# Performance work log

Measured on AMD Instinct MI355X. Metric: run time of the kernel, lower is better.

Reference implementation:

```python
import jax, jax.numpy as jnp
import numpy as np

B, N, D, WIN = 2, 4096, 256, 16


def setup_inputs() -> dict:
    key = jax.random.key(0)
    ks = jax.random.split(key, 10)
    def lin(k, o, i):
        return 0.02 * jax.random.normal(k, (o, i), jnp.float32)
    W = N // WIN
    return {
        "x": 0.5 * jax.random.normal(ks[0], (B, N, D), jnp.float32),
        "embed_qk": jax.random.normal(ks[1], (3, B, W, WIN, WIN, 3), jnp.float32),
        "act_proj_w": lin(ks[2], D, D), "act_proj_b": jnp.zeros((D,), jnp.float32),
        "proj_ln_g": jnp.ones((D,), jnp.float32), "proj_ln_b": jnp.zeros((D,), jnp.float32),
        "conv_w": lin(ks[3], D, D), "conv_b": jnp.zeros((D,), jnp.float32),
        "q_w": lin(ks[4], D, D), "q_b": jnp.zeros((D,), jnp.float32),
        "k_w": lin(ks[5], D, D), "k_b": jnp.zeros((D,), jnp.float32),
        "p_w": lin(ks[6], 1, 3), "p_b": jnp.zeros((1,), jnp.float32),
        "lin_w": lin(ks[7], D, D), "lin_b": jnp.zeros((D,), jnp.float32),
        "norm_g": jnp.ones((D,), jnp.float32), "norm_b": jnp.zeros((D,), jnp.float32),
    }


def _ln(x, g, b, eps=1e-5):
    m = x.mean(-1, keepdims=True)
    v = ((x - m) ** 2).mean(-1, keepdims=True)
    return (x - m) * jax.lax.rsqrt(v + eps) * g + b


def reference(x, embed_qk, act_proj_w, act_proj_b, proj_ln_g, proj_ln_b,
              conv_w, conv_b, q_w, q_b, k_w, k_b, p_w, p_b,
              lin_w, lin_b, norm_g, norm_b):
    # MSMAttentionLayer: gated residual path
    act_res = jax.nn.silu(x @ act_proj_w.T + act_proj_b)          # (B,N,C)
    h = _ln(x, proj_ln_g, proj_ln_b)
    h = jax.nn.silu(h @ conv_w.T + conv_b)                        # 1x1 conv == per-token linear

    # MSMLMultiHeadAttention, stage=1 (window 4x4=16); N % 16 == 0 so add_row_num = 0
    q = jax.nn.elu(h @ q_w.T + q_b) + 1.0
    k = jax.nn.elu(h @ k_w.T + k_b) + 1.0
    v = h
    Bn, Nn, C = h.shape
    Wn = Nn // WIN
    q_win = q.reshape(Bn, Wn, WIN, C)
    k_win = k.reshape(Bn, Wn, WIN, C)
    v_win = v.reshape(Bn, Wn, WIN, C)
    # learned relative-position bias: Linear(3,1) on embed_qk[stage]
    p = (embed_qk[1] @ p_w.T + p_b)[..., 0]
    # second elu+1 feature map (applied on top of q/k which are already elu+1)
    phi_q = jax.nn.elu(q_win) + 1.0
    phi_k = jax.nn.elu(k_win) + 1.0
    # linear-attention style KV aggregation: reduces over windows w
    KV = jnp.einsum('bwmc,bwmd->bmcd', phi_k, v_win)
    att = jnp.einsum('bwnc,bmcd->bwnmd', phi_q, KV) + p[..., None]
    attn_out = att.reshape(Bn, -1, C)[:, :Nn, :]                  # (B,N,C)

    hid = (attn_out * act_res) @ lin_w.T + lin_b
    return _ln(hid + h, norm_g, norm_b)
```

## Files before the change

### kernel.cpp

```cpp
#include <hip/hip_runtime.h>


#define DIM 256
#define NTOK 4096

typedef __attribute__((ext_vector_type(8))) short short8;
typedef __attribute__((ext_vector_type(4))) short short4v;
typedef __attribute__((ext_vector_type(4))) float f32x4;

__device__ __forceinline__ float silu_f(float z) { return z / (1.f + __expf(-z)); }
__device__ __forceinline__ float elu2_f(float z) { return z > 0.f ? z + 2.f : __expf(z) + 1.f; }

__device__ __forceinline__ short f2bf(float f) {
    union { float f; unsigned u; } v; v.f = f;
    unsigned r = v.u + 0x7fffu + ((v.u >> 16) & 1u);
    return (short)(r >> 16);
}
__device__ __forceinline__ float bf2f(short s) {
    union { unsigned u; float f; } v; v.u = ((unsigned)(unsigned short)s) << 16;
    return v.f;
}
__device__ __forceinline__ short8 cvt8(const float* src) {
    const float4 a = *(const float4*)src;
    const float4 c = *(const float4*)(src + 4);
    short8 s;
    s[0] = f2bf(a.x); s[1] = f2bf(a.y); s[2] = f2bf(a.z); s[3] = f2bf(a.w);
    s[4] = f2bf(c.x); s[5] = f2bf(c.y); s[6] = f2bf(c.z); s[7] = f2bf(c.w);
    return s;
}

__device__ __forceinline__ void cast_chunk(const float* __restrict__ src, short* __restrict__ dst,
                                           int chunk, int tid) {
    const int base = chunk * 8192 + tid * 32;
    #pragma unroll
    for (int j = 0; j < 4; ++j)
        *(short8*)(dst + base + j * 8) = cvt8(src + base + j * 8);
}

__global__ __launch_bounds__(256) void fused_dual(
        const float* __restrict__ XF,
        const float* __restrict__ W0f, const float* __restrict__ b0, short* __restrict__ Y0,
        const float* __restrict__ W1f, const float* __restrict__ b1, short* __restrict__ Y1,
        const float* __restrict__ G, const float* __restrict__ Bt,
        const float* __restrict__ Wkf, short* __restrict__ WKB,
        const float* __restrict__ Wqf, short* __restrict__ WQB) {
    const int tid = threadIdx.x;
    if (blockIdx.x >= 64) {
        if (blockIdx.y == 0 && blockIdx.z == 0) {
            const int which = blockIdx.x - 64;
            if (which < 8) cast_chunk(Wkf, WKB, which, tid);
            else cast_chunk(Wqf, WQB, which - 8, tid);
        }
        return;
    }
    __shared__ __align__(16) short Xs[128 * 72];
    __shared__ __align__(16) short Ws[64 * 72];
    __shared__ float stats[128][2];
    const int zz = blockIdx.z;
    const float* Wf = zz ? W1f : W0f;
    const float* bias = zz ? b1 : b0;
    short* Y = zz ? Y1 : Y0;
    const int wv = tid >> 6, l = tid & 63;
    const int lr = l & 15, lk = l >> 4;
    const int r0 = blockIdx.x * 128, c0 = blockIdx.y * 64;
    const int wm = (wv >> 1) * 64, wn = (wv & 1) * 32;

    if (zz) {
        const int prow = tid >> 1, phalf = tid & 1;
        const float* src = XF + (size_t)(r0 + prow) * DIM + phalf * 128;
        float a1 = 0.f, a2 = 0.f;
        #pragma unroll 8
        for (int j = 0; j < 32; ++j) {
            const float4 v = *(const float4*)(src + j * 4);
            a1 += v.x + v.y + v.z + v.w;
            a2 += v.x * v.x + v.y * v.y + v.z * v.z + v.w * v.w;
        }
        a1 += __shfl_xor(a1, 1);
        a2 += __shfl_xor(a2, 1);
        if (!phalf) {
            const float mm = a1 * (1.f / DIM);
            stats[prow][0] = mm;
            stats[prow][1] = rsqrtf(a2 * (1.f / DIM) - mm * mm + 1e-5f);
        }
        __syncthreads();
    }

    f32x4 acc[4][2];
    #pragma unroll
    for (int i = 0; i < 4; ++i)
        #pragma unroll
        for (int j = 0; j < 2; ++j) acc[i][j] = (f32x4){0.f, 0.f, 0.f, 0.f};
    const int sr = tid >> 3, sc = (tid & 7) * 8;
    for (int kt = 0; kt < DIM; kt += 64) {
        float gv[8], bv[8];
        if (zz) {
            const float4 g1 = *(const float4*)(G + kt + sc);
            const float4 g2 = *(const float4*)(G + kt + sc + 4);
            const float4 t1 = *(const float4*)(Bt + kt + sc);
            const float4 t2 = *(const float4*)(Bt + kt + sc + 4);
            gv[0] = g1.x; gv[1] = g1.y; gv[2] = g1.z; gv[3] = g1.w;
            gv[4] = g2.x; gv[5] = g2.y; gv[6] = g2.z; gv[7] = g2.w;
            bv[0] = t1.x; bv[1] = t1.y; bv[2] = t1.z; bv[3] = t1.w;
            bv[4] = t2.x; bv[5] = t2.y; bv[6] = t2.z; bv[7] = t2.w;
        }
        #pragma unroll
        for (int p = 0; p < 4; ++p) {
            const int row = sr + p * 32;
            const float* src = XF + (size_t)(r0 + row) * DIM + kt + sc;
            const float4 a = *(const float4*)src;
            const float4 c = *(const float4*)(src + 4);
            float v[8] = {a.x, a.y, a.z, a.w, c.x, c.y, c.z, c.w};
            short8 s;
            if (zz) {
                const float mm = stats[row][0], rs = stats[row][1];
                #pragma unroll
                for (int j = 0; j < 8; ++j) s[j] = f2bf((v[j] - mm) * rs * gv[j] + bv[j]);
            } else {
                #pragma unroll
                for (int j = 0; j < 8; ++j) s[j] = f2bf(v[j]);
            }
            *(short8*)&Xs[row * 72 + sc] = s;
        }
        #pragma unroll
        for (int p = 0; p < 2; ++p) {
            const int row = sr + p * 32;
            *(short8*)&Ws[row * 72 + sc] = cvt8(Wf + (size_t)(c0 + row) * DIM + kt + sc);
        }
        __syncthreads();
        #pragma unroll
        for (int kc = 0; kc < 2; ++kc) {
            short8 af[4], bfr[2];
            #pragma unroll
            for (int mi = 0; mi < 4; ++mi)
                af[mi] = *(const short8*)&Xs[(wm + mi * 16 + lr) * 72 + kc * 32 + lk * 8];
            #pragma unroll
            for (int ni = 0; ni < 2; ++ni)
                bfr[ni] = *(const short8*)&Ws[(wn + ni * 16 + lr) * 72 + kc * 32 + lk * 8];
            #pragma unroll
            for (int mi = 0; mi < 4; ++mi)
                #pragma unroll
                for (int ni = 0; ni < 2; ++ni)
                    acc[mi][ni] = __builtin_amdgcn_mfma_f32_16x16x32_bf16(af[mi], bfr[ni], acc[mi][ni], 0, 0, 0);
        }
        __syncthreads();
    }
    #pragma unroll
    for (int mi = 0; mi < 4; ++mi)
        #pragma unroll
        for (int ni = 0; ni < 2; ++ni) {
            const int c = c0 + wn + ni * 16 + lr;
            const float bv2 = bias[c];
            #pragma unroll
            for (int i = 0; i < 4; ++i) {
                const int r = r0 + wm + mi * 16 + lk * 4 + i;
                Y[(size_t)r * DIM + c] = f2bf(silu_f(acc[mi][ni][i] + bv2));
            }
        }
}

__global__ __launch_bounds__(256) void gemm_kq(
        const short* __restrict__ H, const short* __restrict__ WKB, const float* __restrict__ bk, short* __restrict__ PK,
        const short* __restrict__ WQB, const float* __restrict__ bq, short* __restrict__ PQ) {
    __shared__ __align__(16) short Xs[128 * 72];
    __shared__ __align__(16) short Ws[64 * 72];
    const int bx = blockIdx.x;
    const bool isq = bx >= 64;
    const short* W = isq ? WQB : WKB;
    const float* bias = isq ? bq : bk;
    short* Y = isq ? PQ : PK;
    const int r0 = (isq ? bx - 64 : bx) * 128;
    const int c0 = blockIdx.y * 64;
    const int tid = threadIdx.x;
    const int wv = tid >> 6, l = tid & 63;
    const int lr = l & 15, lk = l >> 4;
    const int wm = (wv >> 1) * 64, wn = (wv & 1) * 32;
    f32x4 acc[4][2];
    #pragma unroll
    for (int i = 0; i < 4; ++i)
        #pragma unroll
        for (int j = 0; j < 2; ++j) acc[i][j] = (f32x4){0.f, 0.f, 0.f, 0.f};
    const int sr = tid >> 3, sc = (tid & 7) * 8;
    for (int kt = 0; kt < DIM; kt += 64) {
        #pragma unroll
        for (int p = 0; p < 4; ++p) {
            const int row = sr + p * 32;
            int grow = r0 + row;
            if (isq) grow = ((grow >> 8) << 12) + (grow & 255);
            *(short8*)&Xs[row * 72 + sc] = *(const short8*)(H + (size_t)grow * DIM + kt + sc);
        }
        #pragma unroll
        for (int p = 0; p < 2; ++p) {
            const int row = sr + p * 32;
            *(short8*)&Ws[row * 72 + sc] = *(const short8*)(W + (size_t)(c0 + row) * DIM + kt + sc);
        }
        __syncthreads();
        #pragma unroll
        for (int kc = 0; kc < 2; ++kc) {
            short8 af[4], bfr[2];
            #pragma unroll
            for (int mi = 0; mi < 4; ++mi)
                af[mi] = *(const short8*)&Xs[(wm + mi * 16 + lr) * 72 + kc * 32 + lk * 8];
            #pragma unroll
            for (int ni = 0; ni < 2; ++ni)
                bfr[ni] = *(const short8*)&Ws[(wn + ni * 16 + lr) * 72 + kc * 32 + lk * 8];
            #pragma unroll
            for (int mi = 0; mi < 4; ++mi)
                #pragma unroll
                for (int ni = 0; ni < 2; ++ni)
                    acc[mi][ni] = __builtin_amdgcn_mfma_f32_16x16x32_bf16(af[mi], bfr[ni], acc[mi][ni], 0, 0, 0);
        }
        __syncthreads();
    }
    #pragma unroll
    for (int mi = 0; mi < 4; ++mi)
        #pragma unroll
        for (int ni = 0; ni < 2; ++ni) {
            const int c = c0 + wn + ni * 16 + lr;
            const float bv = bias[c];
            #pragma unroll
            for (int i = 0; i < 4; ++i) {
                const int r = r0 + wm + mi * 16 + lk * 4 + i;
                Y[(size_t)r * DIM + c] = f2bf(elu2_f(acc[mi][ni][i] + bv));
            }
        }
}

__global__ __launch_bounds__(256) void kv_mfma(const short* __restrict__ HB, const short* __restrict__ PK,
                                               short* __restrict__ KVT,
                                               const float* __restrict__ Wlf, short* __restrict__ WLB) {
    const int tid = threadIdx.x;
    if (blockIdx.x >= 32) {
        if (blockIdx.y == 0 && blockIdx.z == 0)
            cast_chunk(Wlf, WLB, blockIdx.x - 32, tid);
        return;
    }
    __shared__ __align__(16) short Hs[64 * 68];
    __shared__ __align__(16) short Ps[64 * 68];
    const int bm = blockIdx.x, b = bm >> 4, m = bm & 15;
    const int d0 = blockIdx.y * 64, c0 = blockIdx.z * 64;
    const int wv = tid >> 6, l = tid & 63;
    const int lr = l & 15, lk = l >> 4;
    const int wd = (wv >> 1) * 32, wc = (wv & 1) * 32;
    f32x4 acc[2][2];
    #pragma unroll
    for (int i = 0; i < 2; ++i)
        #pragma unroll
        for (int j = 0; j < 2; ++j) acc[i][j] = (f32x4){0.f, 0.f, 0.f, 0.f};
    const size_t hbase = (size_t)b * NTOK * DIM;
    const int sr = tid >> 3, sc = (tid & 7) * 8;
    for (int kt = 0; kt < 256; kt += 64) {
        #pragma unroll
        for (int p = 0; p < 2; ++p) {
            const int w = sr + p * 32;
            const size_t gg = hbase + (size_t)((kt + w) * 16 + m) * DIM;
            short8 hv = *(const short8*)(HB + gg + d0 + sc);
            short8 pv = *(const short8*)(PK + gg + c0 + sc);
            *(short4v*)&Hs[w * 68 + sc]     = __builtin_shufflevector(hv, hv, 0, 1, 2, 3);
            *(short4v*)&Hs[w * 68 + sc + 4] = __builtin_shufflevector(hv, hv, 4, 5, 6, 7);
            *(short4v*)&Ps[w * 68 + sc]     = __builtin_shufflevector(pv, pv, 0, 1, 2, 3);
            *(short4v*)&Ps[w * 68 + sc + 4] = __builtin_shufflevector(pv, pv, 4, 5, 6, 7);
        }
        __syncthreads();
        #pragma unroll
        for (int kc = 0; kc < 2; ++kc) {
            const int kb = kc * 32 + lk * 8;
            short8 af[2], bfr[2];
            #pragma unroll
            for (int di = 0; di < 2; ++di)
                #pragma unroll
                for (int i = 0; i < 8; ++i)
                    af[di][i] = Hs[(kb + i) * 68 + wd + di * 16 + lr];
            #pragma unroll
            for (int ci = 0; ci < 2; ++ci)
                #pragma unroll
                for (int i = 0; i < 8; ++i)
                    bfr[ci][i] = Ps[(kb + i) * 68 + wc + ci * 16 + lr];
            #pragma unroll
            for (int di = 0; di < 2; ++di)
                #pragma unroll
                for (int ci = 0; ci < 2; ++ci)
                    acc[di][ci] = __builtin_amdgcn_mfma_f32_16x16x32_bf16(af[di], bfr[ci], acc[di][ci], 0, 0, 0);
        }
        __syncthreads();
    }
    #pragma unroll
    for (int di = 0; di < 2; ++di)
        #pragma unroll
        for (int ci = 0; ci < 2; ++ci)
            #pragma unroll
            for (int i = 0; i < 4; ++i) {
                const int d = d0 + wd + di * 16 + lk * 4 + i;
                const int c = c0 + wc + ci * 16 + lr;
                KVT[((size_t)bm * DIM + d) * DIM + c] = f2bf(acc[di][ci][i]);
            }
}

__global__ __launch_bounds__(256) void attlin(
        const short* __restrict__ PQ, const short* __restrict__ KVT,
        const float* __restrict__ emb, const float* __restrict__ pw, const float* __restrict__ pb,
        const short* __restrict__ AR,
        const short* __restrict__ WLB, const float* __restrict__ bl,
        const short* __restrict__ HB, const float* __restrict__ G, const float* __restrict__ Bt,
        float* __restrict__ Y) {
    __shared__ __align__(16) short Qs[32 * 264];
    __shared__ __align__(16) short AGs[32 * 264];
    __shared__ __align__(16) short Bs[256 * 72];
    __shared__ float s1buf[32][2];
    __shared__ float s2buf[32][2];
    const int tid = threadIdx.x;
    const int wv = tid >> 6, l = tid & 63;
    const int lr = l & 15, lk = l >> 4;
    const int bm = blockIdx.x, b = bm >> 4, m = bm & 15;
    const int q0 = blockIdx.y * 32;
    const int wq = (wv >> 1) * 16;
    const int wd = (wv & 1) * 32;
    const int sr = tid >> 3, sc = (tid & 7) * 8;

    #pragma unroll
    for (int p = 0; p < 4; ++p) {
        const int chunk = tid + p * 256;
        const int row = chunk >> 5, cc = (chunk & 31) * 8;
        *(short8*)&Qs[row * 264 + cc] = *(const short8*)(PQ + (size_t)(b * 256 + q0 + row) * DIM + cc);
    }

    f32x4 accA[4][2];
    #pragma unroll
    for (int i = 0; i < 4; ++i)
        #pragma unroll
        for (int j = 0; j < 2; ++j) accA[i][j] = (f32x4){0.f, 0.f, 0.f, 0.f};
    for (int kt = 0; kt < DIM; kt += 64) {
        #pragma unroll
        for (int p = 0; p < 8; ++p) {
            const int row = sr + p * 32;
            *(short8*)&Bs[row * 72 + sc] = *(const short8*)(KVT + ((size_t)bm * DIM + row) * DIM + kt + sc);
        }
        __syncthreads();
        #pragma unroll
        for (int kc = 0; kc < 2; ++kc) {
            const short8 af = *(const short8*)&Qs[(wq + lr) * 264 + kt + kc * 32 + lk * 8];
            #pragma unroll
            for (int dc = 0; dc < 4; ++dc)
                #pragma unroll
                for (int ni = 0; ni < 2; ++ni) {
                    const short8 bfr = *(const short8*)&Bs[(dc * 64 + wd + ni * 16 + lr) * 72 + kc * 32 + lk * 8];
                    accA[dc][ni] = __builtin_amdgcn_mfma_f32_16x16x32_bf16(af, bfr, accA[dc][ni], 0, 0, 0);
                }
        }
        __syncthreads();
    }
    {
        const float pw0 = pw[0], pw1 = pw[1], pw2 = pw[2], pbv = pb[0];
        #pragma unroll
        for (int i = 0; i < 4; ++i) {
            const int rloc = wq + lk * 4 + i;
            const int qr = q0 + rloc;
            const int widx = qr >> 4, nidx = qr & 15;
            const float* e = emb + ((((size_t)(2 + b) * 256 + widx) * 16 + nidx) * 16 + m) * 3;
            const float pv = e[0] * pw0 + e[1] * pw1 + e[2] * pw2 + pbv;
            const int t = qr * 16 + m;
            #pragma unroll
            for (int dc = 0; dc < 4; ++dc)
                #pragma unroll
                for (int ni = 0; ni < 2; ++ni) {
                    const int d = dc * 64 + wd + ni * 16 + lr;
                    const size_t o = ((size_t)b * NTOK + t) * DIM + d;
                    AGs[rloc * 264 + d] = f2bf((accA[dc][ni][i] + pv) * bf2f(AR[o]));
                }
        }
    }
    __syncthreads();

    const int wn2 = (wv & 1) * 128;
    f32x4 accB[8];
    #pragma unroll
    for (int i = 0; i < 8; ++i) accB[i] = (f32x4){0.f, 0.f, 0.f, 0.f};
    for (int kt = 0; kt < DIM; kt += 64) {
        #pragma unroll
        for (int p = 0; p < 8; ++p) {
            const int row = sr + p * 32;
            *(short8*)&Bs[row * 72 + sc] = *(const short8*)(WLB + (size_t)row * DIM + kt + sc);
        }
        __syncthreads();
        #pragma unroll
        for (int kc = 0; kc < 2; ++kc) {
            const short8 af = *(const short8*)&AGs[(wq + lr) * 264 + kt + kc * 32 + lk * 8];
            #pragma unroll
            for (int ni = 0; ni < 8; ++ni) {
                const short8 bfr = *(const short8*)&Bs[(wn2 + ni * 16 + lr) * 72 + kc * 32 + lk * 8];
                accB[ni] = __builtin_amdgcn_mfma_f32_16x16x32_bf16(af, bfr, accB[ni], 0, 0, 0);
            }
        }
        __syncthreads();
    }
    float s1[4] = {0.f, 0.f, 0.f, 0.f}, s2[4] = {0.f, 0.f, 0.f, 0.f};
    #pragma unroll
    for (int ni = 0; ni < 8; ++ni) {
        const int col = wn2 + ni * 16 + lr;
        const float bv = bl[col];
        #pragma unroll
        for (int i = 0; i < 4; ++i) {
            const int rloc = wq + lk * 4 + i;
            const int t = (q0 + rloc) * 16 + m;
            const float z = accB[ni][i] + bv + bf2f(HB[((size_t)b * NTOK + t) * DIM + col]);
            accB[ni][i] = z;
            s1[i] += z; s2[i] += z * z;
        }
    }
    #pragma unroll
    for (int o = 1; o < 16; o <<= 1) {
        #pragma unroll
        for (int i = 0; i < 4; ++i) {
            s1[i] += __shfl_xor(s1[i], o);
            s2[i] += __shfl_xor(s2[i], o);
        }
    }
    if (lr == 0) {
        #pragma unroll
        for (int i = 0; i < 4; ++i) {
            const int rloc = wq + lk * 4 + i;
            s1buf[rloc][wv & 1] = s1[i];
            s2buf[rloc][wv & 1] = s2[i];
        }
    }
    __syncthreads();
    float mean[4], rstd[4];
    #pragma unroll
    for (int i = 0; i < 4; ++i) {
        const int rloc = wq + lk * 4 + i;
        const float t1 = s1buf[rloc][0] + s1buf[rloc][1];
        const float t2 = s2buf[rloc][0] + s2buf[rloc][1];
        const float mm = t1 * (1.f / DIM);
        mean[i] = mm;
        rstd[i] = rsqrtf(t2 * (1.f / DIM) - mm * mm + 1e-5f);
    }
    #pragma unroll
    for (int ni = 0; ni < 8; ++ni) {
        const int col = wn2 + ni * 16 + lr;
        const float gv = G[col], bv2 = Bt[col];
        #pragma unroll
        for (int i = 0; i < 4; ++i) {
            const int rloc = wq + lk * 4 + i;
            const int t = (q0 + rloc) * 16 + m;
            Y[((size_t)b * NTOK + t) * DIM + col] = (accB[ni][i] - mean[i]) * rstd[i] * gv + bv2;
        }
    }
}

extern "C" void kernel_launch(void* const* d_in, const int* in_sizes, int n_in,
                              void* d_out, int out_size, void* d_ws, size_t ws_size,
                              hipStream_t stream) {
    const float* x   = (const float*)d_in[0];
    const float* emb = (const float*)d_in[1];
    const float* Wa  = (const float*)d_in[2];
    const float* ba  = (const float*)d_in[3];
    const float* lng = (const float*)d_in[4];
    const float* lnb = (const float*)d_in[5];
    const float* Wc  = (const float*)d_in[6];
    const float* bc  = (const float*)d_in[7];
    const float* Wq  = (const float*)d_in[8];
    const float* bq  = (const float*)d_in[9];
    const float* Wk  = (const float*)d_in[10];
    const float* bk  = (const float*)d_in[11];
    const float* pw  = (const float*)d_in[12];
    const float* pb  = (const float*)d_in[13];
    const float* Wl  = (const float*)d_in[14];
    const float* bl  = (const float*)d_in[15];
    const float* ng  = (const float*)d_in[16];
    const float* nb  = (const float*)d_in[17];

    char* ws = (char*)d_ws;
    const size_t MB = 1024 * 1024;
    short* h_bf   = (short*)(ws + 0 * MB);
    short* phik   = (short*)(ws + 4 * MB);
    short* phiq   = (short*)(ws + 8 * MB);
    short* kvT    = (short*)(ws + 9 * MB);
    short* act_bf = (short*)(ws + 13 * MB);
    short* Wk_bf  = (short*)(ws + 17 * MB);
    short* Wq_bf  = (short*)(ws + 17 * MB + 128 * 1024);
    short* Wl_bf  = (short*)(ws + 17 * MB + 256 * 1024);

    fused_dual<<<dim3(80, 4, 2), dim3(256), 0, stream>>>(x, Wa, ba, act_bf,
                                                         Wc, bc, h_bf, lng, lnb,
                                                         Wk, Wk_bf, Wq, Wq_bf);
    gemm_kq<<<dim3(68, 4), dim3(256), 0, stream>>>(h_bf, Wk_bf, bk, phik, Wq_bf, bq, phiq);
    kv_mfma<<<dim3(40, 4, 4), dim3(256), 0, stream>>>(h_bf, phik, kvT, Wl, Wl_bf);
    attlin<<<dim3(32, 8), dim3(256), 0, stream>>>(phiq, kvT, emb, pw, pb, act_bf, Wl_bf, bl,
                                                  h_bf, ng, nb, (float*)d_out);
}
```

Baseline: 56.61 us.

## Fuse K and Q projections into KV and attention kernels, drop gemm_kq launch

Removes the separate gemm_kq kernel. phi_k is now computed inside the KV aggregation kernel from shared-memory H tiles and a resident Wk slice, and phi_q is computed at the start of the attention kernel. The Wl bf16 cast moves into the first kernel, so there is one fewer launch and no phi_k/phi_q round trip through global memory. In exchange, kv_fused recomputes the K projection once per d-half (grid z=2) and uses much more shared memory, which may reduce occupancy.

```diff
diff --git a/kernel.cpp b/kernel.cpp
--- a/kernel.cpp
+++ b/kernel.cpp
@@ -28,7 +28,6 @@
     s[4] = f2bf(c.x); s[5] = f2bf(c.y); s[6] = f2bf(c.z); s[7] = f2bf(c.w);
     return s;
 }
-
 __device__ __forceinline__ void cast_chunk(const float* __restrict__ src, short* __restrict__ dst,
                                            int chunk, int tid) {
     const int base = chunk * 8192 + tid * 32;
@@ -43,13 +42,15 @@
         const float* __restrict__ W1f, const float* __restrict__ b1, short* __restrict__ Y1,
         const float* __restrict__ G, const float* __restrict__ Bt,
         const float* __restrict__ Wkf, short* __restrict__ WKB,
-        const float* __restrict__ Wqf, short* __restrict__ WQB) {
+        const float* __restrict__ Wqf, short* __restrict__ WQB,
+        const float* __restrict__ Wlf, short* __restrict__ WLB) {
     const int tid = threadIdx.x;
     if (blockIdx.x >= 64) {
         if (blockIdx.y == 0 && blockIdx.z == 0) {
             const int which = blockIdx.x - 64;
             if (which < 8) cast_chunk(Wkf, WKB, which, tid);
-            else cast_chunk(Wqf, WQB, which - 8, tid);
+            else if (which < 16) cast_chunk(Wqf, WQB, which - 8, tid);
+            else cast_chunk(Wlf, WLB, which - 16, tid);
         }
         return;
     }
@@ -70,8 +71,8 @@
         const float* src = XF + (size_t)(r0 + prow) * DIM + phalf * 128;
         float a1 = 0.f, a2 = 0.f;
         #pragma unroll 8
-        for (int j = 0; j < 32; ++j) {
-            const float4 v = *(const float4*)(src + j * 4);
+        for (int jj = 0; jj < 32; ++jj) {
+            const float4 v = *(const float4*)(src + jj * 4);
             a1 += v.x + v.y + v.z + v.w;
             a2 += v.x * v.x + v.y * v.y + v.z * v.z + v.w * v.w;
         }
@@ -104,8 +105,8 @@
             bv[4] = t2.x; bv[5] = t2.y; bv[6] = t2.z; bv[7] = t2.w;
         }
         #pragma unroll
-        for (int p = 0; p < 4; ++p) {
-            const int row = sr + p * 32;
+        for (int pp = 0; pp < 4; ++pp) {
+            const int row = sr + pp * 32;
             const float* src = XF + (size_t)(r0 + row) * DIM + kt + sc;
             const float4 a = *(const float4*)src;
             const float4 c = *(const float4*)(src + 4);
@@ -122,8 +123,8 @@
             *(short8*)&Xs[row * 72 + sc] = s;
         }
         #pragma unroll
-        for (int p = 0; p < 2; ++p) {
-            const int row = sr + p * 32;
+        for (int pp = 0; pp < 2; ++pp) {
+            const int row = sr + pp * 32;
             *(short8*)&Ws[row * 72 + sc] = cvt8(Wf + (size_t)(c0 + row) * DIM + kt + sc);
         }
         __syncthreads();
@@ -158,153 +159,124 @@
         }
 }
 
-__global__ __launch_bounds__(256) void gemm_kq(
-        const short* __restrict__ H, const short* __restrict__ WKB, const float* __restrict__ bk, short* __restrict__ PK,
-        const short* __restrict__ WQB, const float* __restrict__ bq, short* __restrict__ PQ) {
-    __shared__ __align__(16) short Xs[128 * 72];
-    __shared__ __align__(16) short Ws[64 * 72];
-    const int bx = blockIdx.x;
-    const bool isq = bx >= 64;
-    const short* W = isq ? WQB : WKB;
-    const float* bias = isq ? bq : bk;
-    short* Y = isq ? PQ : PK;
-    const int r0 = (isq ? bx - 64 : bx) * 128;
+__global__ __launch_bounds__(256) void kv_fused(
+        const short* __restrict__ HB, const short* __restrict__ WKB,
+        const float* __restrict__ bk, short* __restrict__ KVT) {
+    __shared__ __align__(16) short Wres[64 * 264];
+    __shared__ __align__(16) short Hs[64 * 264];
+    __shared__ __align__(16) short Ps[64 * 68];
+    const int tid = threadIdx.x;
+    const int bm = blockIdx.x, b = bm >> 4, m = bm & 15;
     const int c0 = blockIdx.y * 64;
-    const int tid = threadIdx.x;
+    const int dh = blockIdx.z * 128;
     const int wv = tid >> 6, l = tid & 63;
     const int lr = l & 15, lk = l >> 4;
-    const int wm = (wv >> 1) * 64, wn = (wv & 1) * 32;
+    const int wd2 = (wv >> 1) * 64, wc2 = (wv & 1) * 32;
+    const int pw_ = (wv >> 1) * 32, pc_ = (wv & 1) * 32;
+
+    #pragma unroll
+    for (int pp = 0; pp < 8; ++pp) {
+        const int chunk = tid + pp * 256;
+        const int row = chunk >> 5, cc = (chunk & 31) * 8;
+        *(short8*)&Wres[row * 264 + cc] = *(const short8*)(WKB + (size_t)(c0 + row) * DIM + cc);
+    }
+
     f32x4 acc[4][2];
     #pragma unroll
     for (int i = 0; i < 4; ++i)
-        #pragma unroll
-        for (int j = 0; j < 2; ++j) acc[i][j] = (f32x4){0.f, 0.f, 0.f, 0.f};
-    const int sr = tid >> 3, sc = (tid & 7) * 8;
-    for (int kt = 0; kt < DIM; kt += 64) {
-        #pragma unroll
-        for (int p = 0; p < 4; ++p) {
-            const int row = sr + p * 32;
-            int grow = r0 + row;
-            if (isq) grow = ((grow >> 8) << 12) + (grow & 255);
-            *(short8*)&Xs[row * 72 + sc] = *(const short8*)(H + (size_t)grow * DIM + kt + sc);
-        }
-        #pragma unroll
-        for (int p = 0; p < 2; ++p) {
-            const int row = sr + p * 32;
-            *(short8*)&Ws[row * 72 + sc] = *(const short8*)(W + (size_t)(c0 + row) * DIM + kt + sc);
-        }
-        __syncthreads();
-        #pragma unroll
-        for (int kc = 0; kc < 2; ++kc) {
-            short8 af[4], bfr[2];
-            #pragma unroll
-            for (int mi = 0; mi < 4; ++mi)
-                af[mi] = *(const short8*)&Xs[(wm + mi * 16 + lr) * 72 + kc * 32 + lk * 8];
-            #pragma unroll
-            for (int ni = 0; ni < 2; ++ni)
-                bfr[ni] = *(const short8*)&Ws[(wn + ni * 16 + lr) * 72 + kc * 32 + lk * 8];
-            #pragma unroll
-            for (int mi = 0; mi < 4; ++mi)
-                #pragma unroll
-                for (int ni = 0; ni < 2; ++ni)
-                    acc[mi][ni] = __builtin_amdgcn_mfma_f32_16x16x32_bf16(af[mi], bfr[ni], acc[mi][ni], 0, 0, 0);
-        }
-        __syncthreads();
-    }
-    #pragma unroll
-    for (int mi = 0; mi < 4; ++mi)
-        #pragma unroll
-        for (int ni = 0; ni < 2; ++ni) {
-            const int c = c0 + wn + ni * 16 + lr;
-            const float bv = bias[c];
-            #pragma unroll
-            for (int i = 0; i < 4; ++i) {
-                const int r = r0 + wm + mi * 16 + lk * 4 + i;
-                Y[(size_t)r * DIM + c] = f2bf(elu2_f(acc[mi][ni][i] + bv));
-            }
-        }
-}
-
-__global__ __launch_bounds__(256) void kv_mfma(const short* __restrict__ HB, const short* __restrict__ PK,
-                                               short* __restrict__ KVT,
-                                               const float* __restrict__ Wlf, short* __restrict__ WLB) {
-    const int tid = threadIdx.x;
-    if (blockIdx.x >= 32) {
-        if (blockIdx.y == 0 && blockIdx.z == 0)
-            cast_chunk(Wlf, WLB, blockIdx.x - 32, tid);
-        return;
-    }
-    __shared__ __align__(16) short Hs[64 * 68];
-    __shared__ __align__(16) short Ps[64 * 68];
-    const int bm = blockIdx.x, b = bm >> 4, m = bm & 15;
-    const int d0 = blockIdx.y * 64, c0 = blockIdx.z * 64;
-    const int wv = tid >> 6, l = tid & 63;
-    const int lr = l & 15, lk = l >> 4;
-    const int wd = (wv >> 1) * 32, wc = (wv & 1) * 32;
-    f32x4 acc[2][2];
-    #pragma unroll
-    for (int i = 0; i < 2; ++i)
         #pragma unroll
         for (int j = 0; j < 2; ++j) acc[i][j] = (f32x4){0.f, 0.f, 0.f, 0.f};
     const size_t hbase = (size_t)b * NTOK * DIM;
-    const int sr = tid >> 3, sc = (tid & 7) * 8;
-    for (int kt = 0; kt < 256; kt += 64) {
-        #pragma unroll
-        for (int p = 0; p < 2; ++p) {
-            const int w = sr + p * 32;
-            const size_t gg = hbase + (size_t)((kt + w) * 16 + m) * DIM;
-            short8 hv = *(const short8*)(HB + gg + d0 + sc);
-            short8 pv = *(const short8*)(PK + gg + c0 + sc);
-            *(short4v*)&Hs[w * 68 + sc]     = __builtin_shufflevector(hv, hv, 0, 1, 2, 3);
-            *(short4v*)&Hs[w * 68 + sc + 4] = __builtin_shufflevector(hv, hv, 4, 5, 6, 7);
-            *(short4v*)&Ps[w * 68 + sc]     = __builtin_shufflevector(pv, pv, 0, 1, 2, 3);
-            *(short4v*)&Ps[w * 68 + sc + 4] = __builtin_shufflevector(pv, pv, 4, 5, 6, 7);
-        }
+    __syncthreads();
+
+    for (int ch = 0; ch < 4; ++ch) {
+        #pragma unroll
+        for (int pp = 0; pp < 8; ++pp) {
+            const int chunk = tid + pp * 256;
+            const int row = chunk >> 5, cc = (chunk & 31) * 8;
+            const size_t g = hbase + (size_t)(((ch * 64 + row) * 16) + m) * DIM + cc;
+            *(short8*)&Hs[row * 264 + cc] = *(const short8*)(HB + g);
+        }
+        __syncthreads();
+        f32x4 pacc[2][2];
+        #pragma unroll
+        for (int i = 0; i < 2; ++i)
+            #pragma unroll
+            for (int j = 0; j < 2; ++j) pacc[i][j] = (f32x4){0.f, 0.f, 0.f, 0.f};
+        for (int kt = 0; kt < DIM; kt += 64) {
+            #pragma unroll
+            for (int kc = 0; kc < 2; ++kc) {
+                short8 af[2], bfr[2];
+                #pragma unroll
+                for (int mi = 0; mi < 2; ++mi)
+                    af[mi] = *(const short8*)&Hs[(pw_ + mi * 16 + lr) * 264 + kt + kc * 32 + lk * 8];
+                #pragma unroll
+                for (int ni = 0; ni < 2; ++ni)
+                    bfr[ni] = *(const short8*)&Wres[(pc_ + ni * 16 + lr) * 264 + kt + kc * 32 + lk * 8];
+                #pragma unroll
+                for (int mi = 0; mi < 2; ++mi)
+                    #pragma unroll
+                    for (int ni = 0; ni < 2; ++ni)
+                        pacc[mi][ni] = __builtin_amdgcn_mfma_f32_16x16x32_bf16(af[mi], bfr[ni], pacc[mi][ni], 0, 0, 0);
+            }
+        }
+        #pragma unroll
+        for (int mi = 0; mi < 2; ++mi)
+            #pragma unroll
+            for (int ni = 0; ni < 2; ++ni) {
+                const int cloc = pc_ + ni * 16 + lr;
+                const float bv = bk[c0 + cloc];
+                #pragma unroll
+                for (int i = 0; i < 4; ++i)
+                    Ps[(pw_ + mi * 16 + lk * 4 + i) * 68 + cloc] = f2bf(elu2_f(pacc[mi][ni][i] + bv));
+            }
         __syncthreads();
         #pragma unroll
         for (int kc = 0; kc < 2; ++kc) {
             const int kb = kc * 32 + lk * 8;
-            short8 af[2], bfr[2];
-            #pragma unroll
-            for (int di = 0; di < 2; ++di)
+            short8 af2[4], bfr2[2];
+            #pragma unroll
+            for (int di = 0; di < 4; ++di)
                 #pragma unroll
                 for (int i = 0; i < 8; ++i)
-                    af[di][i] = Hs[(kb + i) * 68 + wd + di * 16 + lr];
+                    af2[di][i] = Hs[(kb + i) * 264 + dh + wd2 + di * 16 + lr];
             #pragma unroll
             for (int ci = 0; ci < 2; ++ci)
                 #pragma unroll
                 for (int i = 0; i < 8; ++i)
-                    bfr[ci][i] = Ps[(kb + i) * 68 + wc + ci * 16 + lr];
-            #pragma unroll
-            for (int di = 0; di < 2; ++di)
+                    bfr2[ci][i] = Ps[(kb + i) * 68 + wc2 + ci * 16 + lr];
+            #pragma unroll
+            for (int di = 0; di < 4; ++di)
                 #pragma unroll
                 for (int ci = 0; ci < 2; ++ci)
-                    acc[di][ci] = __builtin_amdgcn_mfma_f32_16x16x32_bf16(af[di], bfr[ci], acc[di][ci], 0, 0, 0);
-        }
-        __syncthreads();
-    }
-    #pragma unroll
-    for (int di = 0; di < 2; ++di)
+                    acc[di][ci] = __builtin_amdgcn_mfma_f32_16x16x32_bf16(af2[di], bfr2[ci], acc[di][ci], 0, 0, 0);
+        }
+        __syncthreads();
+    }
+    #pragma unroll
+    for (int di = 0; di < 4; ++di)
         #pragma unroll
         for (int ci = 0; ci < 2; ++ci)
             #pragma unroll
             for (int i = 0; i < 4; ++i) {
-                const int d = d0 + wd + di * 16 + lk * 4 + i;
-                const int c = c0 + wc + ci * 16 + lr;
+                const int d = dh + wd2 + di * 16 + lk * 4 + i;
+                const int c = c0 + wc2 + ci * 16 + lr;
                 KVT[((size_t)bm * DIM + d) * DIM + c] = f2bf(acc[di][ci][i]);
             }
 }
 
-__global__ __launch_bounds__(256) void attlin(
-        const short* __restrict__ PQ, const short* __restrict__ KVT,
+__global__ __launch_bounds__(256) void attlin_fused(
+        const short* __restrict__ HB, const short* __restrict__ WQB, const float* __restrict__ bq,
+        const short* __restrict__ KVT,
         const float* __restrict__ emb, const float* __restrict__ pw, const float* __restrict__ pb,
         const short* __restrict__ AR,
         const short* __restrict__ WLB, const float* __restrict__ bl,
-        const short* __restrict__ HB, const float* __restrict__ G, const float* __restrict__ Bt,
+        const float* __restrict__ G, const float* __restrict__ Bt,
         float* __restrict__ Y) {
     __shared__ __align__(16) short Qs[32 * 264];
     __shared__ __align__(16) short AGs[32 * 264];
     __shared__ __align__(16) short Bs[256 * 72];
+    __shared__ __align__(16) short h32s[32 * 72];
     __shared__ float s1buf[32][2];
     __shared__ float s2buf[32][2];
     const int tid = threadIdx.x;
@@ -314,14 +286,43 @@
     const int q0 = blockIdx.y * 32;
     const int wq = (wv >> 1) * 16;
     const int wd = (wv & 1) * 32;
+    const int wn2 = (wv & 1) * 128;
     const int sr = tid >> 3, sc = (tid & 7) * 8;
 
-    #pragma unroll
-    for (int p = 0; p < 4; ++p) {
-        const int chunk = tid + p * 256;
-        const int row = chunk >> 5, cc = (chunk & 31) * 8;
-        *(short8*)&Qs[row * 264 + cc] = *(const short8*)(PQ + (size_t)(b * 256 + q0 + row) * DIM + cc);
-    }
+    f32x4 acc0[8];
+    #pragma unroll
+    for (int i = 0; i < 8; ++i) acc0[i] = (f32x4){0.f, 0.f, 0.f, 0.f};
+    for (int kt = 0; kt < DIM; kt += 64) {
+        if (sr < 32)
+            *(short8*)&h32s[sr * 72 + sc] = *(const short8*)(HB + (size_t)(b * NTOK + q0 + sr) * DIM + kt + sc);
+        #pragma unroll
+        for (int pp = 0; pp < 8; ++pp) {
+            const int row = sr + pp * 32;
+            *(short8*)&Bs[row * 72 + sc] = *(const short8*)(WQB + (size_t)row * DIM + kt + sc);
+        }
+        __syncthreads();
+        #pragma unroll
+        for (int kc = 0; kc < 2; ++kc) {
+            const short8 af = *(const short8*)&h32s[(wq + lr) * 72 + kc * 32 + lk * 8];
+            #pragma unroll
+            for (int ni = 0; ni < 8; ++ni) {
+                const short8 bfr = *(const short8*)&Bs[(wn2 + ni * 16 + lr) * 72 + kc * 32 + lk * 8];
+                acc0[ni] = __builtin_amdgcn_mfma_f32_16x16x32_bf16(af, bfr, acc0[ni], 0, 0, 0);
+            }
+        }
+        __syncthreads();
+    }
+    #pragma unroll
+    for (int ni = 0; ni < 8; ++ni) {
+        const int col = wn2 + ni * 16 + lr;
+        const float bv = bq[col];
+        #pragma unroll
+        for (int i = 0; i < 4; ++i) {
+            const int rloc = wq + lk * 4 + i;
+            Qs[rloc * 264 + col] = f2bf(elu2_f(acc0[ni][i] + bv));
+        }
+    }
+    __syncthreads();
 
     f32x4 accA[4][2];
     #pragma unroll
@@ -330,8 +331,8 @@
         for (int j = 0; j < 2; ++j) accA[i][j] = (f32x4){0.f, 0.f, 0.f, 0.f};
     for (int kt = 0; kt < DIM; kt += 64) {
         #pragma unroll
-        for (int p = 0; p < 8; ++p) {
-            const int row = sr + p * 32;
+        for (int pp = 0; pp < 8; ++pp) {
+            const int row = sr + pp * 32;
             *(short8*)&Bs[row * 72 + sc] = *(const short8*)(KVT + ((size_t)bm * DIM + row) * DIM + kt + sc);
         }
         __syncthreads();
@@ -370,14 +371,13 @@
     }
     __syncthreads();
 
-    const int wn2 = (wv & 1) * 128;
     f32x4 accB[8];
     #pragma unroll
     for (int i = 0; i < 8; ++i) accB[i] = (f32x4){0.f, 0.f, 0.f, 0.f};
     for (int kt = 0; kt < DIM; kt += 64) {
         #pragma unroll
-        for (int p = 0; p < 8; ++p) {
-            const int row = sr + p * 32;
+        for (int pp = 0; pp < 8; ++pp) {
+            const int row = sr + pp * 32;
             *(short8*)&Bs[row * 72 + sc] = *(const short8*)(WLB + (size_t)row * DIM + kt + sc);
         }
         __syncthreads();
@@ -471,19 +471,16 @@
     char* ws = (char*)d_ws;
     const size_t MB = 1024 * 1024;
     short* h_bf   = (short*)(ws + 0 * MB);
-    short* phik   = (short*)(ws + 4 * MB);
-    short* phiq   = (short*)(ws + 8 * MB);
-    short* kvT    = (short*)(ws + 9 * MB);
-    short* act_bf = (short*)(ws + 13 * MB);
-    short* Wk_bf  = (short*)(ws + 17 * MB);
-    short* Wq_bf  = (short*)(ws + 17 * MB + 128 * 1024);
-    short* Wl_bf  = (short*)(ws + 17 * MB + 256 * 1024);
-
-    fused_dual<<<dim3(80, 4, 2), dim3(256), 0, stream>>>(x, Wa, ba, act_bf,
+    short* kvT    = (short*)(ws + 4 * MB);
+    short* act_bf = (short*)(ws + 8 * MB);
+    short* Wk_bf  = (short*)(ws + 12 * MB);
+    short* Wq_bf  = (short*)(ws + 12 * MB + 128 * 1024);
+    short* Wl_bf  = (short*)(ws + 12 * MB + 256 * 1024);
+
+    fused_dual<<<dim3(88, 4, 2), dim3(256), 0, stream>>>(x, Wa, ba, act_bf,
                                                          Wc, bc, h_bf, lng, lnb,
-                                                         Wk, Wk_bf, Wq, Wq_bf);
-    gemm_kq<<<dim3(68, 4), dim3(256), 0, stream>>>(h_bf, Wk_bf, bk, phik, Wq_bf, bq, phiq);
-    kv_mfma<<<dim3(40, 4, 4), dim3(256), 0, stream>>>(h_bf, phik, kvT, Wl, Wl_bf);
-    attlin<<<dim3(32, 8), dim3(256), 0, stream>>>(phiq, kvT, emb, pw, pb, act_bf, Wl_bf, bl,
-                                                  h_bf, ng, nb, (float*)d_out);
-}
+                                                         Wk, Wk_bf, Wq, Wq_bf, Wl, Wl_bf);
+    kv_fused<<<dim3(32, 4, 2), dim3(256), 0, stream>>>(h_bf, Wk_bf, bk, kvT);
+    attlin_fused<<<dim3(32, 8), dim3(256), 0, stream>>>(h_bf, Wq_bf, bq, kvT, emb, pw, pb,
+                                                        act_bf, Wl_bf, bl, ng, nb, (float*)d_out);
+}
```

Measured after the change: 58.71 us. 1.04x slower.

## Double-buffer LDS and register-prefetch next K tile in fused_dual and gemm_kq GEMMs

Applied to the files above, without the earlier changes.

Both GEMM kernels now keep two LDS buffers and prefetch the next 64-wide K slice from global memory into registers while MFMAs run on the current buffer. This removes one barrier per K step and hides global load latency behind compute. In exchange it doubles LDS use per block and adds register pressure from the prefetched float4/short8 values, which may reduce occupancy.

```diff
diff --git a/kernel.cpp b/kernel.cpp
--- a/kernel.cpp
+++ b/kernel.cpp
@@ -28,7 +28,6 @@
     s[4] = f2bf(c.x); s[5] = f2bf(c.y); s[6] = f2bf(c.z); s[7] = f2bf(c.w);
     return s;
 }
-
 __device__ __forceinline__ void cast_chunk(const float* __restrict__ src, short* __restrict__ dst,
                                            int chunk, int tid) {
     const int base = chunk * 8192 + tid * 32;
@@ -53,8 +52,8 @@
         }
         return;
     }
-    __shared__ __align__(16) short Xs[128 * 72];
-    __shared__ __align__(16) short Ws[64 * 72];
+    __shared__ __align__(16) short Xs[2][128 * 72];
+    __shared__ __align__(16) short Ws[2][64 * 72];
     __shared__ float stats[128][2];
     const int zz = blockIdx.z;
     const float* Wf = zz ? W1f : W0f;
@@ -64,6 +63,7 @@
     const int lr = l & 15, lk = l >> 4;
     const int r0 = blockIdx.x * 128, c0 = blockIdx.y * 64;
     const int wm = (wv >> 1) * 64, wn = (wv & 1) * 32;
+    const int sr = tid >> 3, sc = (tid & 7) * 8;
 
     if (zz) {
         const int prow = tid >> 1, phalf = tid & 1;
@@ -90,59 +90,96 @@
     for (int i = 0; i < 4; ++i)
         #pragma unroll
         for (int j = 0; j < 2; ++j) acc[i][j] = (f32x4){0.f, 0.f, 0.f, 0.f};
-    const int sr = tid >> 3, sc = (tid & 7) * 8;
-    for (int kt = 0; kt < DIM; kt += 64) {
-        float gv[8], bv[8];
+
+    float4 xa[4][2], wa[2][2];
+    #pragma unroll
+    for (int p = 0; p < 4; ++p) {
+        const float* src = XF + (size_t)(r0 + sr + p * 32) * DIM + sc;
+        xa[p][0] = *(const float4*)src;
+        xa[p][1] = *(const float4*)(src + 4);
+    }
+    #pragma unroll
+    for (int p = 0; p < 2; ++p) {
+        const float* src = Wf + (size_t)(c0 + sr + p * 32) * DIM + sc;
+        wa[p][0] = *(const float4*)src;
+        wa[p][1] = *(const float4*)(src + 4);
+    }
+
+    int buf = 0;
+    for (int s = 0; s < 4; ++s) {
+        const int kt = s * 64;
         if (zz) {
             const float4 g1 = *(const float4*)(G + kt + sc);
             const float4 g2 = *(const float4*)(G + kt + sc + 4);
             const float4 t1 = *(const float4*)(Bt + kt + sc);
             const float4 t2 = *(const float4*)(Bt + kt + sc + 4);
-            gv[0] = g1.x; gv[1] = g1.y; gv[2] = g1.z; gv[3] = g1.w;
-            gv[4] = g2.x; gv[5] = g2.y; gv[6] = g2.z; gv[7] = g2.w;
-            bv[0] = t1.x; bv[1] = t1.y; bv[2] = t1.z; bv[3] = t1.w;
-            bv[4] = t2.x; bv[5] = t2.y; bv[6] = t2.z; bv[7] = t2.w;
-        }
-        #pragma unroll
-        for (int p = 0; p < 4; ++p) {
-            const int row = sr + p * 32;
-            const float* src = XF + (size_t)(r0 + row) * DIM + kt + sc;
-            const float4 a = *(const float4*)src;
-            const float4 c = *(const float4*)(src + 4);
-            float v[8] = {a.x, a.y, a.z, a.w, c.x, c.y, c.z, c.w};
-            short8 s;
-            if (zz) {
+            const float gv[8] = {g1.x, g1.y, g1.z, g1.w, g2.x, g2.y, g2.z, g2.w};
+            const float bv[8] = {t1.x, t1.y, t1.z, t1.w, t2.x, t2.y, t2.z, t2.w};
+            #pragma unroll
+            for (int p = 0; p < 4; ++p) {
+                const int row = sr + p * 32;
                 const float mm = stats[row][0], rs = stats[row][1];
-                #pragma unroll
-                for (int j = 0; j < 8; ++j) s[j] = f2bf((v[j] - mm) * rs * gv[j] + bv[j]);
-            } else {
-                #pragma unroll
-                for (int j = 0; j < 8; ++j) s[j] = f2bf(v[j]);
-            }
-            *(short8*)&Xs[row * 72 + sc] = s;
+                const float v[8] = {xa[p][0].x, xa[p][0].y, xa[p][0].z, xa[p][0].w,
+                                    xa[p][1].x, xa[p][1].y, xa[p][1].z, xa[p][1].w};
+                short8 sS;
+                #pragma unroll
+                for (int j = 0; j < 8; ++j) sS[j] = f2bf((v[j] - mm) * rs * gv[j] + bv[j]);
+                *(short8*)&Xs[buf][row * 72 + sc] = sS;
+            }
+        } else {
+            #pragma unroll
+            for (int p = 0; p < 4; ++p) {
+                const int row = sr + p * 32;
+                const float v[8] = {xa[p][0].x, xa[p][0].y, xa[p][0].z, xa[p][0].w,
+                                    xa[p][1].x, xa[p][1].y, xa[p][1].z, xa[p][1].w};
+                short8 sS;
+                #pragma unroll
+                for (int j = 0; j < 8; ++j) sS[j] = f2bf(v[j]);
+                *(short8*)&Xs[buf][row * 72 + sc] = sS;
+            }
         }
         #pragma unroll
         for (int p = 0; p < 2; ++p) {
             const int row = sr + p * 32;
-            *(short8*)&Ws[row * 72 + sc] = cvt8(Wf + (size_t)(c0 + row) * DIM + kt + sc);
-        }
-        __syncthreads();
+            const float v[8] = {wa[p][0].x, wa[p][0].y, wa[p][0].z, wa[p][0].w,
+                                wa[p][1].x, wa[p][1].y, wa[p][1].z, wa[p][1].w};
+            short8 sS;
+            #pragma unroll
+            for (int j = 0; j < 8; ++j) sS[j] = f2bf(v[j]);
+            *(short8*)&Ws[buf][row * 72 + sc] = sS;
+        }
+        __syncthreads();
+        if (s < 3) {
+            const int ktn = kt + 64;
+            #pragma unroll
+            for (int p = 0; p < 4; ++p) {
+                const float* src = XF + (size_t)(r0 + sr + p * 32) * DIM + ktn + sc;
+                xa[p][0] = *(const float4*)src;
+                xa[p][1] = *(const float4*)(src + 4);
+            }
+            #pragma unroll
+            for (int p = 0; p < 2; ++p) {
+                const float* src = Wf + (size_t)(c0 + sr + p * 32) * DIM + ktn + sc;
+                wa[p][0] = *(const float4*)src;
+                wa[p][1] = *(const float4*)(src + 4);
+            }
+        }
         #pragma unroll
         for (int kc = 0; kc < 2; ++kc) {
             short8 af[4], bfr[2];
             #pragma unroll
             for (int mi = 0; mi < 4; ++mi)
-                af[mi] = *(const short8*)&Xs[(wm + mi * 16 + lr) * 72 + kc * 32 + lk * 8];
+                af[mi] = *(const short8*)&Xs[buf][(wm + mi * 16 + lr) * 72 + kc * 32 + lk * 8];
             #pragma unroll
             for (int ni = 0; ni < 2; ++ni)
-                bfr[ni] = *(const short8*)&Ws[(wn + ni * 16 + lr) * 72 + kc * 32 + lk * 8];
+                bfr[ni] = *(const short8*)&Ws[buf][(wn + ni * 16 + lr) * 72 + kc * 32 + lk * 8];
             #pragma unroll
             for (int mi = 0; mi < 4; ++mi)
                 #pragma unroll
                 for (int ni = 0; ni < 2; ++ni)
                     acc[mi][ni] = __builtin_amdgcn_mfma_f32_16x16x32_bf16(af[mi], bfr[ni], acc[mi][ni], 0, 0, 0);
         }
-        __syncthreads();
+        buf ^= 1;
     }
     #pragma unroll
     for (int mi = 0; mi < 4; ++mi)
@@ -161,8 +198,8 @@
 __global__ __launch_bounds__(256) void gemm_kq(
         const short* __restrict__ H, const short* __restrict__ WKB, const float* __restrict__ bk, short* __restrict__ PK,
         const short* __restrict__ WQB, const float* __restrict__ bq, short* __restrict__ PQ) {
-    __shared__ __align__(16) short Xs[128 * 72];
-    __shared__ __align__(16) short Ws[64 * 72];
+    __shared__ __align__(16) short Xs[2][128 * 72];
+    __shared__ __align__(16) short Ws[2][64 * 72];
     const int bx = blockIdx.x;
     const bool isq = bx >= 64;
     const short* W = isq ? WQB : WKB;
@@ -174,42 +211,64 @@
     const int wv = tid >> 6, l = tid & 63;
     const int lr = l & 15, lk = l >> 4;
     const int wm = (wv >> 1) * 64, wn = (wv & 1) * 32;
+    const int sr = tid >> 3, sc = (tid & 7) * 8;
+
+    int growA[4];
+    #pragma unroll
+    for (int p = 0; p < 4; ++p) {
+        int grow = r0 + sr + p * 32;
+        if (isq) grow = ((grow >> 8) << 12) + (grow & 255);
+        growA[p] = grow;
+    }
+
     f32x4 acc[4][2];
     #pragma unroll
     for (int i = 0; i < 4; ++i)
         #pragma unroll
         for (int j = 0; j < 2; ++j) acc[i][j] = (f32x4){0.f, 0.f, 0.f, 0.f};
-    const int sr = tid >> 3, sc = (tid & 7) * 8;
-    for (int kt = 0; kt < DIM; kt += 64) {
-        #pragma unroll
-        for (int p = 0; p < 4; ++p) {
-            const int row = sr + p * 32;
-            int grow = r0 + row;
-            if (isq) grow = ((grow >> 8) << 12) + (grow & 255);
-            *(short8*)&Xs[row * 72 + sc] = *(const short8*)(H + (size_t)grow * DIM + kt + sc);
-        }
-        #pragma unroll
-        for (int p = 0; p < 2; ++p) {
-            const int row = sr + p * 32;
-            *(short8*)&Ws[row * 72 + sc] = *(const short8*)(W + (size_t)(c0 + row) * DIM + kt + sc);
-        }
-        __syncthreads();
+
+    short8 xa[4], wa[2];
+    #pragma unroll
+    for (int p = 0; p < 4; ++p)
+        xa[p] = *(const short8*)(H + (size_t)growA[p] * DIM + sc);
+    #pragma unroll
+    for (int p = 0; p < 2; ++p)
+        wa[p] = *(const short8*)(W + (size_t)(c0 + sr + p * 32) * DIM + sc);
+
+    int buf = 0;
+    for (int s = 0; s < 4; ++s) {
+        #pragma unroll
+        for (int p = 0; p < 4; ++p)
+            *(short8*)&Xs[buf][(sr + p * 32) * 72 + sc] = xa[p];
+        #pragma unroll
+        for (int p = 0; p < 2; ++p)
+            *(short8*)&Ws[buf][(sr + p * 32) * 72 + sc] = wa[p];
+        __syncthreads();
+        if (s < 3) {
+            const int ktn = (s + 1) * 64;
+            #pragma unroll
+            for (int p = 0; p < 4; ++p)
+                xa[p] = *(const short8*)(H + (size_t)growA[p] * DIM + ktn + sc);
+            #pragma unroll
+            for (int p = 0; p < 2; ++p)
+                wa[p] = *(const short8*)(W + (size_t)(c0 + sr + p * 32) * DIM + ktn + sc);
+        }
         #pragma unroll
         for (int kc = 0; kc < 2; ++kc) {
             short8 af[4], bfr[2];
             #pragma unroll
             for (int mi = 0; mi < 4; ++mi)
-                af[mi] = *(const short8*)&Xs[(wm + mi * 16 + lr) * 72 + kc * 32 + lk * 8];
+                af[mi] = *(const short8*)&Xs[buf][(wm + mi * 16 + lr) * 72 + kc * 32 + lk * 8];
             #pragma unroll
             for (int ni = 0; ni < 2; ++ni)
-                bfr[ni] = *(const short8*)&Ws[(wn + ni * 16 + lr) * 72 + kc * 32 + lk * 8];
+                bfr[ni] = *(const short8*)&Ws[buf][(wn + ni * 16 + lr) * 72 + kc * 32 + lk * 8];
             #pragma unroll
             for (int mi = 0; mi < 4; ++mi)
                 #pragma unroll
                 for (int ni = 0; ni < 2; ++ni)
                     acc[mi][ni] = __builtin_amdgcn_mfma_f32_16x16x32_bf16(af[mi], bfr[ni], acc[mi][ni], 0, 0, 0);
         }
-        __syncthreads();
+        buf ^= 1;
     }
     #pragma unroll
     for (int mi = 0; mi < 4; ++mi)
```

Result: faster. 53.86 us (-4.9%).
